# Optimization experiments

Hardware: AMD Instinct MI355X
Metric: run time of the kernel (lower is better)

The kernel has to match this reference:

```python
import jax, jax.numpy as jnp
import numpy as np

N = 50000
E = 800000
DIN = 256
DH = 256
DOUT = 256
R = 8
B = 4


def setup_inputs() -> dict:
    key = jax.random.key(0)
    ks = jax.random.split(key, 12)
    s = 0.05
    return {
        "x": jax.random.normal(ks[0], (N, DIN), jnp.float32),
        "edge_index": jax.random.randint(ks[1], (2, E), 0, N, jnp.int64),
        "edge_type": jax.random.randint(ks[2], (E,), 0, R, jnp.int64),
        "basis1": jax.random.normal(ks[3], (B, DIN, DH), jnp.float32) * s,
        "comp1": jax.random.normal(ks[4], (R, B), jnp.float32) * s,
        "root1": jax.random.normal(ks[5], (DIN, DH), jnp.float32) * s,
        "bias1": jnp.zeros((DH,), jnp.float32),
        "basis2": jax.random.normal(ks[6], (B, DH, DOUT), jnp.float32) * s,
        "comp2": jax.random.normal(ks[7], (R, B), jnp.float32) * s,
        "root2": jax.random.normal(ks[8], (DH, DOUT), jnp.float32) * s,
        "bias2": jnp.zeros((DOUT,), jnp.float32),
    }


def rgcn_conv(x, src, dst, edge_type, basis, comp, root, bias):
    # Basis-decomposed relational conv (PyG RGCNConv, aggr='mean').
    # xb: per-node transform by each basis matrix -> [N, B, out]
    xb = jnp.einsum('ni,bio->nbo', x, basis)
    # Per-edge message: mix bases with relation coefficients -> [E, out]
    msg = jnp.einsum('eb,ebo->eo', comp[edge_type], xb[src])
    # Mean aggregation per (dst, relation): divide each edge by the count of
    # edges of its relation arriving at its destination, then scatter-add.
    key = dst * R + edge_type
    cnt = jax.ops.segment_sum(jnp.ones((msg.shape[0],), x.dtype), key,
                              num_segments=x.shape[0] * R)
    norm = 1.0 / jnp.maximum(cnt, 1.0)
    agg = jax.ops.segment_sum(msg * norm[key][:, None], dst,
                              num_segments=x.shape[0])
    return agg + x @ root + bias


def reference(x, edge_index, edge_type, basis1, comp1, root1, bias1,
              basis2, comp2, root2, bias2):
    src, dst = edge_index[0], edge_index[1]
    h = rgcn_conv(x, src, dst, edge_type, basis1, comp1, root1, bias1)
    h = jax.nn.relu(h)
    # dropout(p=0.4) is identity in eval mode
    out = rgcn_conv(h, src, dst, edge_type, basis2, comp2, root2, bias2)
    return out
```

## Files before the change

kernel.cpp:

```cpp
#include <hip/hip_runtime.h>
#include <hip/hip_bf16.h>

constexpr int N_NODES = 50000;
constexpr int N_EDGES = 800000;
constexpr int R_REL   = 8;
constexpr int BASES   = 4;
constexpr int D       = 256;
constexpr int KZ      = BASES * D;
constexpr int KT      = KZ + D;
constexpr int WSTRIDE = 16;
constexpr int DUMMY_P = 8 << 20;

constexpr int NHI    = (N_NODES + 255) / 256;
constexpr int NS_BLK = 200;
constexpr int CH     = N_EDGES / NS_BLK;

constexpr int NB  = (N_NODES + 255) / 256;
constexpr int CB4 = (N_NODES * 128) / 1024;
constexpr int WKB = KT / 64;
constexpr int WB  = (N_NODES * WSTRIDE) / 256;
constexpr int CAP = N_EDGES + N_NODES * 8;
constexpr int FB4 = (CAP + 1023) / 1024;

typedef __attribute__((ext_vector_type(8))) short bf16x8;
typedef __attribute__((ext_vector_type(4))) float f32x4;

__device__ inline float bfu_lo(unsigned u) { return __uint_as_float(u << 16); }
__device__ inline float bfu_hi(unsigned u) { return __uint_as_float(u & 0xFFFF0000u); }
__device__ inline unsigned short f2bu(float f) {
  __hip_bfloat16 h = __float2bfloat16(f);
  return *reinterpret_cast<unsigned short*>(&h);
}
__device__ inline void store_out(float* p, float v) { *p = v; }
__device__ inline void store_out(__hip_bfloat16* p, float v) { *p = __float2bfloat16(v); }

__device__ inline void gload_lds16(void* lds, const void* g) {
  __builtin_amdgcn_global_load_lds(
      (const __attribute__((address_space(1))) unsigned*)g,
      (__attribute__((address_space(3))) unsigned*)lds, 16, 0, 0);
}

__global__ __launch_bounds__(256) void prep_kernel(
    const int* __restrict__ ei, const int* __restrict__ et,
    int* __restrict__ gcoarse,
    const float* __restrict__ x, unsigned* __restrict__ x2,
    const float* __restrict__ basis1, const float* __restrict__ root1,
    __hip_bfloat16* __restrict__ WT1,
    const float* __restrict__ basis2, const float* __restrict__ root2,
    __hip_bfloat16* __restrict__ WT2,
    int* __restrict__ packed) {
  __shared__ __hip_bfloat16 tile[16][256];
  __shared__ int hist[NHI];
  int bid = blockIdx.x;
  int tid = threadIdx.x;

  if (bid < NS_BLK) {
    if (tid < NHI) hist[tid] = 0;
    __syncthreads();
    int start = bid * CH, end = start + CH;
    for (int i = start + tid; i < end; i += 256) {
      int dst = ei[N_EDGES + i];
      atomicAdd(&hist[dst >> 8], 1);
    }
    __syncthreads();
    if (tid < NHI && hist[tid] > 0) atomicAdd(&gcoarse[tid], hist[tid]);
    return;
  }
  bid -= NS_BLK;
  if (bid < CB4) {
    int idx = (bid * 256 + tid) * 4;
    const float* px = x + (size_t)idx * 2;
    float4 a = *(const float4*)(px);
    float4 b = *(const float4*)(px + 4);
    uint4 o;
    o.x = (unsigned)f2bu(a.x) | ((unsigned)f2bu(a.y) << 16);
    o.y = (unsigned)f2bu(a.z) | ((unsigned)f2bu(a.w) << 16);
    o.z = (unsigned)f2bu(b.x) | ((unsigned)f2bu(b.y) << 16);
    o.w = (unsigned)f2bu(b.z) | ((unsigned)f2bu(b.w) << 16);
    *(uint4*)(x2 + idx) = o;
    return;
  }
  bid -= CB4;
  if (bid < 2 * WKB) {
    const float* basis = (bid < WKB) ? basis1 : basis2;
    const float* root  = (bid < WKB) ? root1 : root2;
    __hip_bfloat16* WT = (bid < WKB) ? WT1 : WT2;
    int wb = (bid < WKB) ? bid : bid - WKB;
    int k0 = wb * 64;
#pragma unroll
    for (int pass = 0; pass < 4; pass++) {
      int kp = k0 + pass * 16;
#pragma unroll
      for (int r = 0; r < 16; r++) {
        int k = kp + r;
        const float* srow = (k < KZ)
            ? basis + ((size_t)(k & 3) * D + (k >> 2)) * D
            : root + (size_t)(k - KZ) * D;
        tile[r][tid] = __float2bfloat16(srow[tid]);
      }
      __syncthreads();
      __hip_bfloat16* dst = WT + (size_t)tid * KT + kp;
#pragma unroll
      for (int c = 0; c < 2; c++) {
        union { short s[8]; int4 v; } u;
#pragma unroll
        for (int r = 0; r < 8; r++)
          u.s[r] = *reinterpret_cast<short*>(&tile[c * 8 + r][tid]);
        *(int4*)(dst + c * 8) = u.v;
      }
      __syncthreads();
    }
    return;
  }
  bid -= 2 * WKB;
  {
    int i = (bid * 256 + tid) * 4;
    if (i < CAP) {
      int4 f = make_int4(DUMMY_P, DUMMY_P, DUMMY_P, DUMMY_P);
      *(int4*)(packed + i) = f;
    }
  }
}

__global__ __launch_bounds__(256) void coarse_prefix_kernel(
    const int* __restrict__ gcoarse, int* __restrict__ gbase,
    int* __restrict__ gcur) {
  __shared__ int sd[256];
  int tid = threadIdx.x;
  int v = (tid < NHI) ? gcoarse[tid] : 0;
  sd[tid] = v;
  __syncthreads();
  for (int off = 1; off < 256; off <<= 1) {
    int t = (tid >= off) ? sd[tid - off] : 0;
    __syncthreads();
    sd[tid] += t;
    __syncthreads();
  }
  if (tid < NHI) {
    int b = sd[tid] - v;
    gbase[tid] = b;
    gcur[tid] = b;
  }
}

__global__ __launch_bounds__(256) void coarse_scatter_kernel(
    const int* __restrict__ ei, const int* __restrict__ et,
    int* __restrict__ gcur, int* __restrict__ coarse) {
  __shared__ int hist[NHI];
  __shared__ int lbase[NHI];
  __shared__ int lcnt[NHI];
  int bid = blockIdx.x;
  int tid = threadIdx.x;
  if (tid < NHI) { hist[tid] = 0; lcnt[tid] = 0; }
  __syncthreads();
  int start = bid * CH, end = start + CH;
  for (int i = start + tid; i < end; i += 256)
    atomicAdd(&hist[ei[N_EDGES + i] >> 8], 1);
  __syncthreads();
  if (tid < NHI) lbase[tid] = atomicAdd(&gcur[tid], hist[tid]);
  __syncthreads();
  for (int i = start + tid; i < end; i += 256) {
    int src = ei[i];
    int dst = ei[N_EDGES + i];
    int rt  = et[i];
    int bin = dst >> 8;
    int rank = atomicAdd(&lcnt[bin], 1);
    coarse[lbase[bin] + rank] = src | (rt << 16) | ((dst & 255) << 19);
  }
}

__global__ __launch_bounds__(256) void fine_hist_kernel(
    const int* __restrict__ coarse, const int* __restrict__ gbase,
    const int* __restrict__ gcoarse, int* __restrict__ cnt,
    int* __restrict__ lestart, int* __restrict__ btot) {
  __shared__ int c2[256 * R_REL];
  __shared__ int sd[256];
  int b = blockIdx.x;
  int tid = threadIdx.x;
#pragma unroll
  for (int k = tid; k < 256 * R_REL; k += 256) c2[k] = 0;
  __syncthreads();
  int base = gbase[b], n_e = gcoarse[b];
  for (int i = tid; i < n_e; i += 256) {
    int e = coarse[base + i];
    int key = ((e >> 19) & 255) * R_REL + ((e >> 16) & 7);
    atomicAdd(&c2[key], 1);
  }
  __syncthreads();
  int nodebase = b * 256;
#pragma unroll
  for (int k = tid; k < 256 * R_REL; k += 256) {
    int n = nodebase + (k >> 3);
    if (n < N_NODES) cnt[n * R_REL + (k & 7)] = c2[k];
  }
  int d = 0;
#pragma unroll
  for (int r = 0; r < R_REL; r++) d += c2[tid * R_REL + r];
  int dp = (d + 7) & ~7;
  sd[tid] = dp;
  __syncthreads();
  for (int off = 1; off < 256; off <<= 1) {
    int t = (tid >= off) ? sd[tid - off] : 0;
    __syncthreads();
    sd[tid] += t;
    __syncthreads();
  }
  lestart[b * 256 + tid] = sd[tid] - dp;
  if (tid == 255) btot[b] = sd[255];
}

__global__ __launch_bounds__(256) void btot_prefix_kernel(
    const int* __restrict__ btot, int* __restrict__ bbase,
    int* __restrict__ estart) {
  __shared__ int sd[256];
  int tid = threadIdx.x;
  int v = (tid < NHI) ? btot[tid] : 0;
  sd[tid] = v;
  __syncthreads();
  for (int off = 1; off < 256; off <<= 1) {
    int t = (tid >= off) ? sd[tid - off] : 0;
    __syncthreads();
    sd[tid] += t;
    __syncthreads();
  }
  if (tid < NHI) bbase[tid] = sd[tid] - v;
  if (tid == NHI - 1) estart[N_NODES] = sd[tid];
}

__global__ __launch_bounds__(256) void finalize_kernel(
    const int* __restrict__ bbase, const int* __restrict__ lestart,
    int* __restrict__ estart, const int* __restrict__ cnt,
    const float* __restrict__ comp1, float4* __restrict__ wtab1,
    const float* __restrict__ comp2, float4* __restrict__ wtab2) {
  int bid = blockIdx.x;
  int tid = threadIdx.x;
  if (bid < NB) {
    int n = bid * 256 + tid;
    if (n < N_NODES) estart[n] = bbase[n >> 8] + lestart[n];
    return;
  }
  bid -= NB;
  {
    const float* comp = (bid < WB) ? comp1 : comp2;
    float4* wtab = (bid < WB) ? wtab1 : wtab2;
    int lb = (bid < WB) ? bid : bid - WB;
    int idx = lb * 256 + tid;
    int r = idx & (WSTRIDE - 1);
    int n = idx >> 4;
    float4 w = make_float4(0.f, 0.f, 0.f, 0.f);
    if (r < R_REL) {
      int c = cnt[n * R_REL + r];
      float inv = 1.0f / (float)(c > 0 ? c : 1);
      w.x = comp[r * BASES + 0] * inv;
      w.y = comp[r * BASES + 1] * inv;
      w.z = comp[r * BASES + 2] * inv;
      w.w = comp[r * BASES + 3] * inv;
    }
    wtab[idx] = w;
  }
}

__global__ __launch_bounds__(256) void fine_scatter_kernel(
    const int* __restrict__ coarse, const int* __restrict__ gbase,
    const int* __restrict__ gcoarse, const int* __restrict__ bbase,
    const int* __restrict__ lestart, int* __restrict__ packed) {
  __shared__ int lest[256];
  __shared__ int lcur[256];
  int b = blockIdx.x;
  int tid = threadIdx.x;
  lest[tid] = lestart[b * 256 + tid];
  lcur[tid] = 0;
  __syncthreads();
  int base = gbase[b], n_e = gcoarse[b];
  int sb = bbase[b];
  for (int i = tid; i < n_e; i += 256) {
    int e = coarse[base + i];
    int lo = (e >> 19) & 255;
    int rank = atomicAdd(&lcur[lo], 1);
    packed[sb + lest[lo] + rank] = (e & 0xFFFF) | (((e >> 16) & 7) << 20);
  }
}

__device__ inline float2 pfma(float s, float2 a, float2 c) {
  c.x = fmaf(s, a.x, c.x);
  c.y = fmaf(s, a.y, c.y);
  return c;
}

__device__ inline void edge_fma(float2 acc[BASES][2], uint2 v, float4 w) {
  float2 a01 = make_float2(bfu_lo(v.x), bfu_hi(v.x));
  float2 a23 = make_float2(bfu_lo(v.y), bfu_hi(v.y));
  acc[0][0] = pfma(w.x, a01, acc[0][0]); acc[0][1] = pfma(w.x, a23, acc[0][1]);
  acc[1][0] = pfma(w.y, a01, acc[1][0]); acc[1][1] = pfma(w.y, a23, acc[1][1]);
  acc[2][0] = pfma(w.z, a01, acc[2][0]); acc[2][1] = pfma(w.z, a23, acc[2][1]);
  acc[3][0] = pfma(w.w, a01, acc[3][0]); acc[3][1] = pfma(w.w, a23, acc[3][1]);
}

__global__ __launch_bounds__(256) void aggregate_kernel(
    const unsigned* __restrict__ x2,
    const int* __restrict__ packed,
    const int* __restrict__ estart,
    const float4* __restrict__ wtab,
    __hip_bfloat16* __restrict__ zA)
{
  int tid = threadIdx.x;
  int lane = tid & 63;
  int n = __builtin_amdgcn_readfirstlane(blockIdx.x * 4 + (tid >> 6));
  int s = __builtin_amdgcn_readfirstlane(estart[n]);
  int e = __builtin_amdgcn_readfirstlane(estart[n + 1]);
  const int voff = lane * 2;
  const float4* wt = wtab + (size_t)n * WSTRIDE;

  float2 acc[BASES][2] = {};

  for (int base = s; base < e; base += 8) {
    int4 q0 = *(const int4*)(packed + base);
    int4 q1 = *(const int4*)(packed + base + 4);
    int p0 = __builtin_amdgcn_readfirstlane(q0.x);
    int p1 = __builtin_amdgcn_readfirstlane(q0.y);
    int p2 = __builtin_amdgcn_readfirstlane(q0.z);
    int p3 = __builtin_amdgcn_readfirstlane(q0.w);
    int p4 = __builtin_amdgcn_readfirstlane(q1.x);
    int p5 = __builtin_amdgcn_readfirstlane(q1.y);
    int p6 = __builtin_amdgcn_readfirstlane(q1.z);
    int p7 = __builtin_amdgcn_readfirstlane(q1.w);
    const unsigned* r0 = x2 + ((size_t)(p0 & 0xFFFFF) << 7);
    const unsigned* r1 = x2 + ((size_t)(p1 & 0xFFFFF) << 7);
    const unsigned* r2 = x2 + ((size_t)(p2 & 0xFFFFF) << 7);
    const unsigned* r3 = x2 + ((size_t)(p3 & 0xFFFFF) << 7);
    const unsigned* r4 = x2 + ((size_t)(p4 & 0xFFFFF) << 7);
    const unsigned* r5 = x2 + ((size_t)(p5 & 0xFFFFF) << 7);
    const unsigned* r6 = x2 + ((size_t)(p6 & 0xFFFFF) << 7);
    const unsigned* r7 = x2 + ((size_t)(p7 & 0xFFFFF) << 7);
    uint2 v0 = *(const uint2*)(r0 + voff);
    uint2 v1 = *(const uint2*)(r1 + voff);
    uint2 v2 = *(const uint2*)(r2 + voff);
    uint2 v3 = *(const uint2*)(r3 + voff);
    uint2 v4 = *(const uint2*)(r4 + voff);
    uint2 v5 = *(const uint2*)(r5 + voff);
    uint2 v6 = *(const uint2*)(r6 + voff);
    uint2 v7 = *(const uint2*)(r7 + voff);
    float4 w0 = wt[p0 >> 20];
    float4 w1 = wt[p1 >> 20];
    float4 w2 = wt[p2 >> 20];
    float4 w3 = wt[p3 >> 20];
    float4 w4 = wt[p4 >> 20];
    float4 w5 = wt[p5 >> 20];
    float4 w6 = wt[p6 >> 20];
    float4 w7 = wt[p7 >> 20];
    edge_fma(acc, v0, w0);
    edge_fma(acc, v1, w1);
    edge_fma(acc, v2, w2);
    edge_fma(acc, v3, w3);
    edge_fma(acc, v4, w4);
    edge_fma(acc, v5, w5);
    edge_fma(acc, v6, w6);
    edge_fma(acc, v7, w7);
  }

  union { short s[8]; int4 v; } u0, u1;
#pragma unroll
  for (int b = 0; b < BASES; b++) {
    u0.s[b]     = (short)f2bu(acc[b][0].x);
    u0.s[4 + b] = (short)f2bu(acc[b][0].y);
    u1.s[b]     = (short)f2bu(acc[b][1].x);
    u1.s[4 + b] = (short)f2bu(acc[b][1].y);
  }
  __hip_bfloat16* zrow = zA + (size_t)n * KZ;
  *(int4*)(zrow + 16 * lane) = u0.v;
  *(int4*)(zrow + 16 * lane + 8) = u1.v;
}

#define BM 128
#define BN 256
#define BK 32

template <bool RELU, typename OutT>
__global__ __launch_bounds__(512) void gemm_kernel(
    const __hip_bfloat16* __restrict__ Az,
    const __hip_bfloat16* __restrict__ Aself,
    const __hip_bfloat16* __restrict__ Bt,
    const float* __restrict__ bias, OutT* __restrict__ C, int M) {
  __shared__ __align__(16) __hip_bfloat16 As[BM * BK];
  __shared__ __align__(16) __hip_bfloat16 Bs[BN * BK];
  int tid = threadIdx.x;
  int m0 = blockIdx.x * BM;
  int wave = tid >> 6, lane = tid & 63;
  int wm = wave & 1, wn = wave >> 1;
  int l15 = lane & 15, quad = lane >> 4;

  int colS = (lane & 3) * 8;
  int rowA = wave * 16 + (lane >> 2);
  int grA  = min(m0 + rowA, M - 1);
  const __hip_bfloat16* gAz = Az + (size_t)grA * KZ + colS;
  const __hip_bfloat16* gAs = Aself + (size_t)grA * D + colS;
  const __hip_bfloat16* gB0 = Bt + (size_t)(wave * 32 + (lane >> 2)) * KT + colS;
  const __hip_bfloat16* gB1 = gB0 + 16 * KT;
  __hip_bfloat16* lA  = As + wave * 512;
  __hip_bfloat16* lB0 = Bs + wave * 1024;
  __hip_bfloat16* lB1 = Bs + wave * 1024 + 512;

  f32x4 acc[4][4] = {};

  for (int k0 = 0; k0 < KT; k0 += BK) {
    const __hip_bfloat16* srcA = (k0 < KZ) ? (gAz + k0) : (gAs + (k0 - KZ));
    gload_lds16(lA, srcA);
    gload_lds16(lB0, gB0 + k0);
    gload_lds16(lB1, gB1 + k0);
    __syncthreads();

    bf16x8 af[4], bfr[4];
#pragma unroll
    for (int mt = 0; mt < 4; mt++)
      af[mt] = *(const bf16x8*)(As + (wm * 64 + mt * 16 + l15) * BK + quad * 8);
#pragma unroll
    for (int nt = 0; nt < 4; nt++)
      bfr[nt] = *(const bf16x8*)(Bs + (wn * 64 + nt * 16 + l15) * BK + quad * 8);
#pragma unroll
    for (int mt = 0; mt < 4; mt++)
#pragma unroll
      for (int nt = 0; nt < 4; nt++)
        acc[mt][nt] = __builtin_amdgcn_mfma_f32_16x16x32_bf16(
            af[mt], bfr[nt], acc[mt][nt], 0, 0, 0);
    __syncthreads();
  }

#pragma unroll
  for (int nt = 0; nt < 4; nt++) {
    int cg = wn * 64 + nt * 16 + l15;
    float bv = bias[cg];
#pragma unroll
    for (int mt = 0; mt < 4; mt++) {
#pragma unroll
      for (int r = 0; r < 4; r++) {
        int rg = m0 + wm * 64 + mt * 16 + quad * 4 + r;
        if (rg < M) {
          float v = acc[mt][nt][r] + bv;
          if (RELU) v = fmaxf(v, 0.f);
          store_out(C + (size_t)rg * D + cg, v);
        }
      }
    }
  }
}

static inline char* carve(char*& p, size_t bytes) {
  char* r = p;
  p += (bytes + 255) & ~(size_t)255;
  return r;
}

extern "C" void kernel_launch(void* const* d_in, const int* in_sizes, int n_in,
                              void* d_out, int out_size, void* d_ws,
                              size_t ws_size, hipStream_t stream) {
  const float* x      = (const float*)d_in[0];
  const int*   ei     = (const int*)d_in[1];
  const int*   et     = (const int*)d_in[2];
  const float* basis1 = (const float*)d_in[3];
  const float* comp1  = (const float*)d_in[4];
  const float* root1  = (const float*)d_in[5];
  const float* bias1  = (const float*)d_in[6];
  const float* basis2 = (const float*)d_in[7];
  const float* comp2  = (const float*)d_in[8];
  const float* root2  = (const float*)d_in[9];
  const float* bias2  = (const float*)d_in[10];
  float* out = (float*)d_out;

  char* ws = (char*)d_ws;
  int* cnt     = (int*)carve(ws, (size_t)N_NODES * R_REL * 4);
  int* estart  = (int*)carve(ws, (size_t)(N_NODES + 1) * 4);
  int* coarse  = (int*)carve(ws, (size_t)N_EDGES * 4);
  int* lestart = (int*)carve(ws, (size_t)NHI * 256 * 4);
  int* gcoarse = (int*)carve(ws, 256 * 4);
  int* gbase   = (int*)carve(ws, 256 * 4);
  int* gcur    = (int*)carve(ws, 256 * 4);
  int* btot    = (int*)carve(ws, 256 * 4);
  int* bbase   = (int*)carve(ws, 256 * 4);
  int* packed  = (int*)carve(ws, (size_t)CAP * 4);
  float4* wtab1 = (float4*)carve(ws, (size_t)N_NODES * WSTRIDE * 16);
  float4* wtab2 = (float4*)carve(ws, (size_t)N_NODES * WSTRIDE * 16);
  __hip_bfloat16* WT1 = (__hip_bfloat16*)carve(ws, (size_t)D * KT * 2);
  __hip_bfloat16* WT2 = (__hip_bfloat16*)carve(ws, (size_t)D * KT * 2);
  unsigned* xb = (unsigned*)carve(ws, (size_t)N_NODES * D * 2);
  __hip_bfloat16* h = (__hip_bfloat16*)carve(ws, (size_t)N_NODES * D * 2);
  __hip_bfloat16* zA = (__hip_bfloat16*)carve(ws, (size_t)N_NODES * KZ * 2);

  hipMemsetAsync(gcoarse, 0, 256 * 4, stream);

  prep_kernel<<<NS_BLK + CB4 + 2 * WKB + FB4, 256, 0, stream>>>(
      ei, et, gcoarse, x, xb, basis1, root1, WT1, basis2, root2, WT2, packed);
  coarse_prefix_kernel<<<1, 256, 0, stream>>>(gcoarse, gbase, gcur);
  coarse_scatter_kernel<<<NS_BLK, 256, 0, stream>>>(ei, et, gcur, coarse);
  fine_hist_kernel<<<NHI, 256, 0, stream>>>(coarse, gbase, gcoarse, cnt,
                                            lestart, btot);
  btot_prefix_kernel<<<1, 256, 0, stream>>>(btot, bbase, estart);
  finalize_kernel<<<NB + 2 * WB, 256, 0, stream>>>(bbase, lestart, estart, cnt,
                                                   comp1, wtab1, comp2, wtab2);
  fine_scatter_kernel<<<NHI, 256, 0, stream>>>(coarse, gbase, gcoarse, bbase,
                                               lestart, packed);

  dim3 ggrid((N_NODES + BM - 1) / BM, 1);
  const int AB = (N_NODES + 3) / 4;

  aggregate_kernel<<<AB, 256, 0, stream>>>(xb, packed, estart, wtab1, zA);
  gemm_kernel<true, __hip_bfloat16><<<ggrid, 512, 0, stream>>>(
      zA, (const __hip_bfloat16*)xb, WT1, bias1, h, N_NODES);

  aggregate_kernel<<<AB, 256, 0, stream>>>((const unsigned*)h, packed, estart,
                                           wtab2, zA);
  gemm_kernel<false, float><<<ggrid, 512, 0, stream>>>(
      zA, h, WT2, bias2, out, N_NODES);
}
```

Measured before the change: 443.9 us.

## Precompute per-edge weights and double-buffer GEMM LDS staging

Fine scatter now writes each edge's normalized basis coefficients into dense per-edge arrays, so aggregation reads them sequentially instead of indexing the per-node relation table. The GEMM uses two LDS buffers and issues the next K-tile's async global-to-LDS loads before computing the current tile, using explicit vmcnt waits and raw barriers. The trade-off is extra memory traffic for zeroing and writing two large per-edge weight arrays, plus doubled LDS use in the GEMM, which may reduce occupancy.

Result: slower. 468.2 us (+5.5%).

```diff
diff --git a/kernel.cpp b/kernel.cpp
--- a/kernel.cpp
+++ b/kernel.cpp
@@ -21,6 +21,7 @@
 constexpr int WB  = (N_NODES * WSTRIDE) / 256;
 constexpr int CAP = N_EDGES + N_NODES * 8;
 constexpr int FB4 = (CAP + 1023) / 1024;
+constexpr int WF4 = (CAP + 1023) / 1024;
 
 typedef __attribute__((ext_vector_type(8))) short bf16x8;
 typedef __attribute__((ext_vector_type(4))) float f32x4;
@@ -48,7 +49,8 @@
     __hip_bfloat16* __restrict__ WT1,
     const float* __restrict__ basis2, const float* __restrict__ root2,
     __hip_bfloat16* __restrict__ WT2,
-    int* __restrict__ packed) {
+    int* __restrict__ packed,
+    float4* __restrict__ wedge1, float4* __restrict__ wedge2) {
   __shared__ __hip_bfloat16 tile[16][256];
   __shared__ int hist[NHI];
   int bid = blockIdx.x;
@@ -113,11 +115,22 @@
     return;
   }
   bid -= 2 * WKB;
-  {
+  if (bid < FB4) {
     int i = (bid * 256 + tid) * 4;
     if (i < CAP) {
       int4 f = make_int4(DUMMY_P, DUMMY_P, DUMMY_P, DUMMY_P);
       *(int4*)(packed + i) = f;
+    }
+    return;
+  }
+  bid -= FB4;
+  {
+    float4* wz = (bid < WF4) ? wedge1 : wedge2;
+    int lb = (bid < WF4) ? bid : bid - WF4;
+    int i = (lb * 256 + tid) * 4;
+    if (i < CAP) {
+      float4 z = make_float4(0.f, 0.f, 0.f, 0.f);
+      wz[i] = z; wz[i + 1] = z; wz[i + 2] = z; wz[i + 3] = z;
     }
   }
 }
@@ -263,7 +276,10 @@
 __global__ __launch_bounds__(256) void fine_scatter_kernel(
     const int* __restrict__ coarse, const int* __restrict__ gbase,
     const int* __restrict__ gcoarse, const int* __restrict__ bbase,
-    const int* __restrict__ lestart, int* __restrict__ packed) {
+    const int* __restrict__ lestart,
+    const float4* __restrict__ wtab1, const float4* __restrict__ wtab2,
+    int* __restrict__ packed,
+    float4* __restrict__ wedge1, float4* __restrict__ wedge2) {
   __shared__ int lest[256];
   __shared__ int lcur[256];
   int b = blockIdx.x;
@@ -276,8 +292,13 @@
   for (int i = tid; i < n_e; i += 256) {
     int e = coarse[base + i];
     int lo = (e >> 19) & 255;
+    int rt = (e >> 16) & 7;
     int rank = atomicAdd(&lcur[lo], 1);
-    packed[sb + lest[lo] + rank] = (e & 0xFFFF) | (((e >> 16) & 7) << 20);
+    int pos = sb + lest[lo] + rank;
+    packed[pos] = (e & 0xFFFF) | (rt << 20);
+    int widx = (b * 256 + lo) * WSTRIDE + rt;
+    wedge1[pos] = wtab1[widx];
+    wedge2[pos] = wtab2[widx];
   }
 }
 
@@ -299,8 +320,8 @@
 __global__ __launch_bounds__(256) void aggregate_kernel(
     const unsigned* __restrict__ x2,
     const int* __restrict__ packed,
+    const float4* __restrict__ wedge,
     const int* __restrict__ estart,
-    const float4* __restrict__ wtab,
     __hip_bfloat16* __restrict__ zA)
 {
   int tid = threadIdx.x;
@@ -309,7 +330,6 @@
   int s = __builtin_amdgcn_readfirstlane(estart[n]);
   int e = __builtin_amdgcn_readfirstlane(estart[n + 1]);
   const int voff = lane * 2;
-  const float4* wt = wtab + (size_t)n * WSTRIDE;
 
   float2 acc[BASES][2] = {};
 
@@ -340,14 +360,14 @@
     uint2 v5 = *(const uint2*)(r5 + voff);
     uint2 v6 = *(const uint2*)(r6 + voff);
     uint2 v7 = *(const uint2*)(r7 + voff);
-    float4 w0 = wt[p0 >> 20];
-    float4 w1 = wt[p1 >> 20];
-    float4 w2 = wt[p2 >> 20];
-    float4 w3 = wt[p3 >> 20];
-    float4 w4 = wt[p4 >> 20];
-    float4 w5 = wt[p5 >> 20];
-    float4 w6 = wt[p6 >> 20];
-    float4 w7 = wt[p7 >> 20];
+    float4 w0 = wedge[base + 0];
+    float4 w1 = wedge[base + 1];
+    float4 w2 = wedge[base + 2];
+    float4 w3 = wedge[base + 3];
+    float4 w4 = wedge[base + 4];
+    float4 w5 = wedge[base + 5];
+    float4 w6 = wedge[base + 6];
+    float4 w7 = wedge[base + 7];
     edge_fma(acc, v0, w0);
     edge_fma(acc, v1, w1);
     edge_fma(acc, v2, w2);
@@ -381,8 +401,8 @@
     const __hip_bfloat16* __restrict__ Aself,
     const __hip_bfloat16* __restrict__ Bt,
     const float* __restrict__ bias, OutT* __restrict__ C, int M) {
-  __shared__ __align__(16) __hip_bfloat16 As[BM * BK];
-  __shared__ __align__(16) __hip_bfloat16 Bs[BN * BK];
+  __shared__ __align__(16) __hip_bfloat16 As[2][BM * BK];
+  __shared__ __align__(16) __hip_bfloat16 Bs[2][BN * BK];
   int tid = threadIdx.x;
   int m0 = blockIdx.x * BM;
   int wave = tid >> 6, lane = tid & 63;
@@ -396,33 +416,43 @@
   const __hip_bfloat16* gAs = Aself + (size_t)grA * D + colS;
   const __hip_bfloat16* gB0 = Bt + (size_t)(wave * 32 + (lane >> 2)) * KT + colS;
   const __hip_bfloat16* gB1 = gB0 + 16 * KT;
-  __hip_bfloat16* lA  = As + wave * 512;
-  __hip_bfloat16* lB0 = Bs + wave * 1024;
-  __hip_bfloat16* lB1 = Bs + wave * 1024 + 512;
 
   f32x4 acc[4][4] = {};
 
+  auto stage = [&](int buf, int k0) {
+    const __hip_bfloat16* srcA = (k0 < KZ) ? (gAz + k0) : (gAs + (k0 - KZ));
+    gload_lds16(As[buf] + wave * 512, srcA);
+    gload_lds16(Bs[buf] + wave * 1024, gB0 + k0);
+    gload_lds16(Bs[buf] + wave * 1024 + 512, gB1 + k0);
+  };
+
+  stage(0, 0);
+  int cur = 0;
   for (int k0 = 0; k0 < KT; k0 += BK) {
-    const __hip_bfloat16* srcA = (k0 < KZ) ? (gAz + k0) : (gAs + (k0 - KZ));
-    gload_lds16(lA, srcA);
-    gload_lds16(lB0, gB0 + k0);
-    gload_lds16(lB1, gB1 + k0);
-    __syncthreads();
+    if (k0 + BK < KT) {
+      stage(cur ^ 1, k0 + BK);
+      asm volatile("s_waitcnt vmcnt(3)" ::: "memory");
+    } else {
+      asm volatile("s_waitcnt vmcnt(0)" ::: "memory");
+    }
+    __builtin_amdgcn_s_barrier();
+    __builtin_amdgcn_sched_barrier(0);
 
     bf16x8 af[4], bfr[4];
 #pragma unroll
     for (int mt = 0; mt < 4; mt++)
-      af[mt] = *(const bf16x8*)(As + (wm * 64 + mt * 16 + l15) * BK + quad * 8);
+      af[mt] = *(const bf16x8*)(As[cur] + (wm * 64 + mt * 16 + l15) * BK + quad * 8);
 #pragma unroll
     for (int nt = 0; nt < 4; nt++)
-      bfr[nt] = *(const bf16x8*)(Bs + (wn * 64 + nt * 16 + l15) * BK + quad * 8);
+      bfr[nt] = *(const bf16x8*)(Bs[cur] + (wn * 64 + nt * 16 + l15) * BK + quad * 8);
 #pragma unroll
     for (int mt = 0; mt < 4; mt++)
 #pragma unroll
       for (int nt = 0; nt < 4; nt++)
         acc[mt][nt] = __builtin_amdgcn_mfma_f32_16x16x32_bf16(
             af[mt], bfr[nt], acc[mt][nt], 0, 0, 0);
-    __syncthreads();
+    __builtin_amdgcn_s_barrier();
+    cur ^= 1;
   }
 
 #pragma unroll
@@ -477,6 +507,8 @@
   int* btot    = (int*)carve(ws, 256 * 4);
   int* bbase   = (int*)carve(ws, 256 * 4);
   int* packed  = (int*)carve(ws, (size_t)CAP * 4);
+  float4* wedge1 = (float4*)carve(ws, (size_t)CAP * 16);
+  float4* wedge2 = (float4*)carve(ws, (size_t)CAP * 16);
   float4* wtab1 = (float4*)carve(ws, (size_t)N_NODES * WSTRIDE * 16);
   float4* wtab2 = (float4*)carve(ws, (size_t)N_NODES * WSTRIDE * 16);
   __hip_bfloat16* WT1 = (__hip_bfloat16*)carve(ws, (size_t)D * KT * 2);
@@ -487,8 +519,9 @@
 
   hipMemsetAsync(gcoarse, 0, 256 * 4, stream);
 
-  prep_kernel<<<NS_BLK + CB4 + 2 * WKB + FB4, 256, 0, stream>>>(
-      ei, et, gcoarse, x, xb, basis1, root1, WT1, basis2, root2, WT2, packed);
+  prep_kernel<<<NS_BLK + CB4 + 2 * WKB + FB4 + 2 * WF4, 256, 0, stream>>>(
+      ei, et, gcoarse, x, xb, basis1, root1, WT1, basis2, root2, WT2,
+      packed, wedge1, wedge2);
   coarse_prefix_kernel<<<1, 256, 0, stream>>>(gcoarse, gbase, gcur);
   coarse_scatter_kernel<<<NS_BLK, 256, 0, stream>>>(ei, et, gcur, coarse);
   fine_hist_kernel<<<NHI, 256, 0, stream>>>(coarse, gbase, gcoarse, cnt,
@@ -497,17 +530,18 @@
   finalize_kernel<<<NB + 2 * WB, 256, 0, stream>>>(bbase, lestart, estart, cnt,
                                                    comp1, wtab1, comp2, wtab2);
   fine_scatter_kernel<<<NHI, 256, 0, stream>>>(coarse, gbase, gcoarse, bbase,
-                                               lestart, packed);
+                                               lestart, wtab1, wtab2,
+                                               packed, wedge1, wedge2);
 
   dim3 ggrid((N_NODES + BM - 1) / BM, 1);
   const int AB = (N_NODES + 3) / 4;
 
-  aggregate_kernel<<<AB, 256, 0, stream>>>(xb, packed, estart, wtab1, zA);
+  aggregate_kernel<<<AB, 256, 0, stream>>>(xb, packed, wedge1, estart, zA);
   gemm_kernel<true, __hip_bfloat16><<<ggrid, 512, 0, stream>>>(
       zA, (const __hip_bfloat16*)xb, WT1, bias1, h, N_NODES);
 
-  aggregate_kernel<<<AB, 256, 0, stream>>>((const unsigned*)h, packed, estart,
-                                           wtab2, zA);
+  aggregate_kernel<<<AB, 256, 0, stream>>>((const unsigned*)h, packed, wedge2,
+                                           estart, zA);
   gemm_kernel<false, float><<<ggrid, 512, 0, stream>>>(
       zA, h, WT2, bias2, out, N_NODES);
 }
```

## Double-buffer GEMM LDS loads and fold finalize kernel into histogram/scatter kernels

Applied to the files above, without the earlier changes.

The GEMM now stages the next K tile into a second LDS buffer with async global-to-LDS loads while computing the current one, using explicit vmcnt waits and barriers in place of __syncthreads. This is meant to hide global-load latency behind the MFMA work. Separately, the finalize kernel is removed: the weight tables are built directly in fine_hist_kernel from the shared-memory counts, and estart is written in fine_scatter_kernel. That drops one launch and the cnt buffer round trip. It doubles GEMM LDS use, which may lower occupancy, and relies on the vmcnt counts matching the issued loads.

Measured after the change: 441.6 us. No clear change (-0.5%).

```diff
diff --git a/kernel.cpp b/kernel.cpp
--- a/kernel.cpp
+++ b/kernel.cpp
@@ -15,10 +15,8 @@
 constexpr int NS_BLK = 200;
 constexpr int CH     = N_EDGES / NS_BLK;
 
-constexpr int NB  = (N_NODES + 255) / 256;
 constexpr int CB4 = (N_NODES * 128) / 1024;
 constexpr int WKB = KT / 64;
-constexpr int WB  = (N_NODES * WSTRIDE) / 256;
 constexpr int CAP = N_EDGES + N_NODES * 8;
 constexpr int FB4 = (CAP + 1023) / 1024;
 
@@ -171,7 +169,9 @@
 
 __global__ __launch_bounds__(256) void fine_hist_kernel(
     const int* __restrict__ coarse, const int* __restrict__ gbase,
-    const int* __restrict__ gcoarse, int* __restrict__ cnt,
+    const int* __restrict__ gcoarse,
+    const float* __restrict__ comp1, float4* __restrict__ wtab1,
+    const float* __restrict__ comp2, float4* __restrict__ wtab2,
     int* __restrict__ lestart, int* __restrict__ btot) {
   __shared__ int c2[256 * R_REL];
   __shared__ int sd[256];
@@ -188,10 +188,27 @@
   }
   __syncthreads();
   int nodebase = b * 256;
-#pragma unroll
-  for (int k = tid; k < 256 * R_REL; k += 256) {
-    int n = nodebase + (k >> 3);
-    if (n < N_NODES) cnt[n * R_REL + (k & 7)] = c2[k];
+  for (int k = tid; k < 256 * WSTRIDE; k += 256) {
+    int lo = k >> 4, r = k & (WSTRIDE - 1);
+    int n = nodebase + lo;
+    if (n < N_NODES) {
+      float4 w1 = make_float4(0.f, 0.f, 0.f, 0.f);
+      float4 w2 = w1;
+      if (r < R_REL) {
+        int c = c2[lo * R_REL + r];
+        float inv = 1.0f / (float)(c > 0 ? c : 1);
+        w1.x = comp1[r * BASES + 0] * inv;
+        w1.y = comp1[r * BASES + 1] * inv;
+        w1.z = comp1[r * BASES + 2] * inv;
+        w1.w = comp1[r * BASES + 3] * inv;
+        w2.x = comp2[r * BASES + 0] * inv;
+        w2.y = comp2[r * BASES + 1] * inv;
+        w2.z = comp2[r * BASES + 2] * inv;
+        w2.w = comp2[r * BASES + 3] * inv;
+      }
+      wtab1[(size_t)n * WSTRIDE + r] = w1;
+      wtab2[(size_t)n * WSTRIDE + r] = w2;
+    }
   }
   int d = 0;
 #pragma unroll
@@ -227,52 +244,24 @@
   if (tid == NHI - 1) estart[N_NODES] = sd[tid];
 }
 
-__global__ __launch_bounds__(256) void finalize_kernel(
-    const int* __restrict__ bbase, const int* __restrict__ lestart,
-    int* __restrict__ estart, const int* __restrict__ cnt,
-    const float* __restrict__ comp1, float4* __restrict__ wtab1,
-    const float* __restrict__ comp2, float4* __restrict__ wtab2) {
-  int bid = blockIdx.x;
-  int tid = threadIdx.x;
-  if (bid < NB) {
-    int n = bid * 256 + tid;
-    if (n < N_NODES) estart[n] = bbase[n >> 8] + lestart[n];
-    return;
-  }
-  bid -= NB;
-  {
-    const float* comp = (bid < WB) ? comp1 : comp2;
-    float4* wtab = (bid < WB) ? wtab1 : wtab2;
-    int lb = (bid < WB) ? bid : bid - WB;
-    int idx = lb * 256 + tid;
-    int r = idx & (WSTRIDE - 1);
-    int n = idx >> 4;
-    float4 w = make_float4(0.f, 0.f, 0.f, 0.f);
-    if (r < R_REL) {
-      int c = cnt[n * R_REL + r];
-      float inv = 1.0f / (float)(c > 0 ? c : 1);
-      w.x = comp[r * BASES + 0] * inv;
-      w.y = comp[r * BASES + 1] * inv;
-      w.z = comp[r * BASES + 2] * inv;
-      w.w = comp[r * BASES + 3] * inv;
-    }
-    wtab[idx] = w;
-  }
-}
-
 __global__ __launch_bounds__(256) void fine_scatter_kernel(
     const int* __restrict__ coarse, const int* __restrict__ gbase,
     const int* __restrict__ gcoarse, const int* __restrict__ bbase,
-    const int* __restrict__ lestart, int* __restrict__ packed) {
+    const int* __restrict__ lestart, int* __restrict__ estart,
+    int* __restrict__ packed) {
   __shared__ int lest[256];
   __shared__ int lcur[256];
   int b = blockIdx.x;
   int tid = threadIdx.x;
+  int sb = bbase[b];
   lest[tid] = lestart[b * 256 + tid];
   lcur[tid] = 0;
+  {
+    int n = b * 256 + tid;
+    if (n < N_NODES) estart[n] = sb + lest[tid];
+  }
   __syncthreads();
   int base = gbase[b], n_e = gcoarse[b];
-  int sb = bbase[b];
   for (int i = tid; i < n_e; i += 256) {
     int e = coarse[base + i];
     int lo = (e >> 19) & 255;
@@ -381,8 +370,8 @@
     const __hip_bfloat16* __restrict__ Aself,
     const __hip_bfloat16* __restrict__ Bt,
     const float* __restrict__ bias, OutT* __restrict__ C, int M) {
-  __shared__ __align__(16) __hip_bfloat16 As[BM * BK];
-  __shared__ __align__(16) __hip_bfloat16 Bs[BN * BK];
+  __shared__ __align__(16) __hip_bfloat16 As[2][BM * BK];
+  __shared__ __align__(16) __hip_bfloat16 Bs[2][BN * BK];
   int tid = threadIdx.x;
   int m0 = blockIdx.x * BM;
   int wave = tid >> 6, lane = tid & 63;
@@ -396,33 +385,43 @@
   const __hip_bfloat16* gAs = Aself + (size_t)grA * D + colS;
   const __hip_bfloat16* gB0 = Bt + (size_t)(wave * 32 + (lane >> 2)) * KT + colS;
   const __hip_bfloat16* gB1 = gB0 + 16 * KT;
-  __hip_bfloat16* lA  = As + wave * 512;
-  __hip_bfloat16* lB0 = Bs + wave * 1024;
-  __hip_bfloat16* lB1 = Bs + wave * 1024 + 512;
 
   f32x4 acc[4][4] = {};
 
+  auto stage = [&](int buf, int k0) {
+    const __hip_bfloat16* srcA = (k0 < KZ) ? (gAz + k0) : (gAs + (k0 - KZ));
+    gload_lds16(As[buf] + wave * 512, srcA);
+    gload_lds16(Bs[buf] + wave * 1024, gB0 + k0);
+    gload_lds16(Bs[buf] + wave * 1024 + 512, gB1 + k0);
+  };
+
+  stage(0, 0);
+  int cur = 0;
   for (int k0 = 0; k0 < KT; k0 += BK) {
-    const __hip_bfloat16* srcA = (k0 < KZ) ? (gAz + k0) : (gAs + (k0 - KZ));
-    gload_lds16(lA, srcA);
-    gload_lds16(lB0, gB0 + k0);
-    gload_lds16(lB1, gB1 + k0);
-    __syncthreads();
+    if (k0 + BK < KT) {
+      stage(cur ^ 1, k0 + BK);
+      asm volatile("s_waitcnt vmcnt(3)" ::: "memory");
+    } else {
+      asm volatile("s_waitcnt vmcnt(0)" ::: "memory");
+    }
+    __builtin_amdgcn_s_barrier();
+    __builtin_amdgcn_sched_barrier(0);
 
     bf16x8 af[4], bfr[4];
 #pragma unroll
     for (int mt = 0; mt < 4; mt++)
-      af[mt] = *(const bf16x8*)(As + (wm * 64 + mt * 16 + l15) * BK + quad * 8);
+      af[mt] = *(const bf16x8*)(As[cur] + (wm * 64 + mt * 16 + l15) * BK + quad * 8);
 #pragma unroll
     for (int nt = 0; nt < 4; nt++)
-      bfr[nt] = *(const bf16x8*)(Bs + (wn * 64 + nt * 16 + l15) * BK + quad * 8);
+      bfr[nt] = *(const bf16x8*)(Bs[cur] + (wn * 64 + nt * 16 + l15) * BK + quad * 8);
 #pragma unroll
     for (int mt = 0; mt < 4; mt++)
 #pragma unroll
       for (int nt = 0; nt < 4; nt++)
         acc[mt][nt] = __builtin_amdgcn_mfma_f32_16x16x32_bf16(
             af[mt], bfr[nt], acc[mt][nt], 0, 0, 0);
-    __syncthreads();
+    __builtin_amdgcn_s_barrier();
+    cur ^= 1;
   }
 
 #pragma unroll
@@ -467,7 +466,6 @@
   float* out = (float*)d_out;
 
   char* ws = (char*)d_ws;
-  int* cnt     = (int*)carve(ws, (size_t)N_NODES * R_REL * 4);
   int* estart  = (int*)carve(ws, (size_t)(N_NODES + 1) * 4);
   int* coarse  = (int*)carve(ws, (size_t)N_EDGES * 4);
   int* lestart = (int*)carve(ws, (size_t)NHI * 256 * 4);
@@ -491,13 +489,12 @@
       ei, et, gcoarse, x, xb, basis1, root1, WT1, basis2, root2, WT2, packed);
   coarse_prefix_kernel<<<1, 256, 0, stream>>>(gcoarse, gbase, gcur);
   coarse_scatter_kernel<<<NS_BLK, 256, 0, stream>>>(ei, et, gcur, coarse);
-  fine_hist_kernel<<<NHI, 256, 0, stream>>>(coarse, gbase, gcoarse, cnt,
+  fine_hist_kernel<<<NHI, 256, 0, stream>>>(coarse, gbase, gcoarse,
+                                            comp1, wtab1, comp2, wtab2,
                                             lestart, btot);
   btot_prefix_kernel<<<1, 256, 0, stream>>>(btot, bbase, estart);
-  finalize_kernel<<<NB + 2 * WB, 256, 0, stream>>>(bbase, lestart, estart, cnt,
-                                                   comp1, wtab1, comp2, wtab2);
   fine_scatter_kernel<<<NHI, 256, 0, stream>>>(coarse, gbase, gcoarse, bbase,
-                                               lestart, packed);
+                                               lestart, estart, packed);
 
   dim3 ggrid((N_NODES + BM - 1) / BM, 1);
   const int AB = (N_NODES + 3) / 4;
```
